# Optimization experiments

Hardware: AMD Instinct MI355X
Metric: run time of the kernel (lower is better)

## Reference

```python
import jax, jax.numpy as jnp
import numpy as np

N = 100000
E = 1600000
D = 64        # HID_NODE_ENC == HID_EDGE_ENC
H = 128       # HIDDEN_NODE_ONE
EPS = 1e-5
NEG_SLOPE = 0.01


def _xavier(key, shape):
    fan_in, fan_out = shape[0], shape[1]
    limit = float(np.sqrt(6.0 / (fan_in + fan_out)))
    return jax.random.uniform(key, shape, jnp.float32, -limit, limit)


def setup_inputs() -> dict:
    key = jax.random.key(0)
    ks = jax.random.split(key, 10)
    x = jax.random.normal(ks[0], (N, D), jnp.float32)
    edge_index = jax.random.randint(ks[1], (2, E), 0, N, jnp.int64)
    edge_attr = jax.random.normal(ks[2], (E, D), jnp.float32)
    u = jax.random.normal(ks[3], (1, 16), jnp.float32)
    batch = jnp.zeros((N,), jnp.int64)
    b_init = jnp.float32(0.01)
    params = {
        # node_mlp_1: Lin(128->128), LeakyReLU, BN(128), Lin(128->128)
        "W1": _xavier(ks[4], (2 * D, H)), "b1": jnp.full((H,), b_init),
        "g1": jnp.ones((H,), jnp.float32), "be1": jnp.zeros((H,), jnp.float32),
        "W2": _xavier(ks[5], (H, H)), "b2": jnp.full((H,), b_init),
        # node_mlp_2: Lin(192->128), LeakyReLU, BN(128), Lin(128->64)
        "W3": _xavier(ks[6], (H + D, H)), "b3": jnp.full((H,), b_init),
        "g2": jnp.ones((H,), jnp.float32), "be2": jnp.zeros((H,), jnp.float32),
        "W4": _xavier(ks[7], (H, D)), "b4": jnp.full((D,), b_init),
    }
    return {"x": x, "edge_index": edge_index, "edge_attr": edge_attr,
            "u": u, "batch": batch, **params}


def _bn(h, gamma, beta):
    # BatchNorm1d in training mode: biased batch statistics
    mean = jnp.mean(h, axis=0)
    var = jnp.mean(jnp.square(h - mean), axis=0)
    return (h - mean) * jax.lax.rsqrt(var + EPS) * gamma + beta


def reference(x, edge_index, edge_attr, u, batch,
              W1, b1, g1, be1, W2, b2,
              W3, b3, g2, be2, W4, b4):
    row, col = edge_index[0], edge_index[1]
    # gather + concat: [E, 2D]
    h = jnp.concatenate([x[row], edge_attr], axis=1)
    # node_mlp_1
    h = jax.nn.leaky_relu(h @ W1 + b1, NEG_SLOPE)
    h = _bn(h, g1, be1)
    h = h @ W2 + b2                       # [E, H]
    # scatter_add by destination node
    agg = jax.ops.segment_sum(h, col, num_segments=x.shape[0])  # [N, H]
    # concat with node feats, node_mlp_2
    h2 = jnp.concatenate([x, agg], axis=1)  # [N, H+D]
    h2 = jax.nn.leaky_relu(h2 @ W3 + b3, NEG_SLOPE)
    h2 = _bn(h2, g2, be2)
    return h2 @ W4 + b4                    # [N, D]
```

## Files before the change

### kernel.cpp

```cpp
#include <hip/hip_runtime.h>

#define NN 100000
#define NE 1600000
#define NTILE_E (NE / 128)
#define NTILE_N 782

typedef __attribute__((ext_vector_type(4))) float f32x4;
typedef __attribute__((ext_vector_type(8))) short s16x8;

__device__ __forceinline__ unsigned short f2bf(float f) {
  unsigned u = __builtin_bit_cast(unsigned, f);
  u = (u + 0x7FFFu + ((u >> 16) & 1u)) >> 16;
  return (unsigned short)u;
}
__device__ __forceinline__ void pack4(float4 v, unsigned short* dst) {
  ushort4 h;
  h.x = f2bf(v.x); h.y = f2bf(v.y); h.z = f2bf(v.z); h.w = f2bf(v.w);
  *(ushort4*)dst = h;
}

__global__ void k0_prep(const float* __restrict__ W1, const float* __restrict__ W3,
                        unsigned short* __restrict__ W1bT, unsigned short* __restrict__ W3bT) {
  int i = blockIdx.x * 256 + threadIdx.x;
  if (i < 16384) {
    int n = i >> 7, k = i & 127;
    W1bT[i] = f2bf(W1[k * 128 + n]);
  } else if (i < 16384 + 24576) {
    int j = i - 16384;
    int n = j / 192, k = j % 192;
    W3bT[j] = f2bf(W3[k * 128 + n]);
  }
}

__global__ __launch_bounds__(256, 2) void k1_edge(
    const float* __restrict__ x, const int* __restrict__ eidx,
    const float* __restrict__ ea, const unsigned short* __restrict__ W1bT,
    const float* __restrict__ b1,
    float* __restrict__ S, float* __restrict__ cnt, float* __restrict__ stat1) {
  __shared__ unsigned short At[128][136];
  __shared__ int rIdx[128];
  __shared__ int cIdx[128];
  __shared__ float sred[256];

  const int tid = threadIdx.x;
  const int wave = tid >> 6, lane = tid & 63;
  const int l15 = lane & 15, quad = lane >> 4;
  const int rowbase = (wave >> 1) * 64;
  const int colbase = (wave & 1) * 64;

  s16x8 bfrag[4][4];
#pragma unroll
  for (int ct = 0; ct < 4; ct++)
#pragma unroll
    for (int ks = 0; ks < 4; ks++)
      bfrag[ct][ks] = *(const s16x8*)(W1bT + (colbase + ct * 16 + l15) * 128 + ks * 32 + quad * 8);

  float b1j[4];
#pragma unroll
  for (int ct = 0; ct < 4; ct++) b1j[ct] = b1[colbase + ct * 16 + l15];

  float lsum[4] = {0, 0, 0, 0}, lsq[4] = {0, 0, 0, 0};

  for (int tile = blockIdx.x; tile < NTILE_E; tile += gridDim.x) {
    const int eb = tile * 128;
    __syncthreads();
    if (tid < 128) { rIdx[tid] = eidx[eb + tid]; cIdx[tid] = eidx[NE + eb + tid]; }
    __syncthreads();
#pragma unroll
    for (int i = 0; i < 8; i++) {
      int idx = tid + i * 256; int e = idx >> 4, c = idx & 15;
      float4 v = ((const float4*)x)[(size_t)rIdx[e] * 16 + c];
      pack4(v, &At[e][c * 4]);
    }
#pragma unroll
    for (int i = 0; i < 8; i++) {
      int idx = tid + i * 256; int e = idx >> 4, c = idx & 15;
      float4 v = ((const float4*)ea)[(size_t)(eb + e) * 16 + c];
      pack4(v, &At[e][64 + c * 4]);
    }
    __syncthreads();
    if (tid < 128) atomicAdd(&cnt[cIdx[tid]], 1.0f);

    f32x4 acc[4][4];
#pragma unroll
    for (int rt = 0; rt < 4; rt++)
#pragma unroll
      for (int ct = 0; ct < 4; ct++) acc[rt][ct] = (f32x4){0.f, 0.f, 0.f, 0.f};

#pragma unroll
    for (int ks = 0; ks < 4; ks++) {
      s16x8 af[4];
#pragma unroll
      for (int rt = 0; rt < 4; rt++)
        af[rt] = *(const s16x8*)&At[rowbase + rt * 16 + l15][ks * 32 + quad * 8];
#pragma unroll
      for (int rt = 0; rt < 4; rt++)
#pragma unroll
        for (int ct = 0; ct < 4; ct++)
          acc[rt][ct] = __builtin_amdgcn_mfma_f32_16x16x32_bf16(af[rt], bfrag[ct][ks], acc[rt][ct], 0, 0, 0);
    }

#pragma unroll
    for (int rt = 0; rt < 4; rt++) {
#pragma unroll
      for (int r = 0; r < 4; r++) {
        const int er = rowbase + rt * 16 + quad * 4 + r;
        float* Srow = S + (size_t)cIdx[er] * 128;
#pragma unroll
        for (int ct = 0; ct < 4; ct++) {
          float v = acc[rt][ct][r] + b1j[ct];
          v = v > 0.0f ? v : 0.01f * v;
          lsum[ct] += v; lsq[ct] += v * v;
          atomicAdd(Srow + colbase + ct * 16 + l15, v);
        }
      }
    }
  }

  sred[tid] = 0.0f;
  __syncthreads();
#pragma unroll
  for (int ct = 0; ct < 4; ct++) {
    float s = lsum[ct], q = lsq[ct];
    s += __shfl_down(s, 32); q += __shfl_down(q, 32);
    s += __shfl_down(s, 16); q += __shfl_down(q, 16);
    if (lane < 16) {
      atomicAdd(&sred[colbase + ct * 16 + l15], s);
      atomicAdd(&sred[128 + colbase + ct * 16 + l15], q);
    }
  }
  __syncthreads();
  atomicAdd(&stat1[tid], sred[tid]);
}

__global__ void k2_fold1(const float* __restrict__ stat1, const float* __restrict__ g1,
                         const float* __restrict__ be1, const float* __restrict__ W2,
                         const float* __restrict__ b2,
                         unsigned short* __restrict__ W2pT, float* __restrict__ v128) {
  __shared__ float s1s[128], t1s[128];
  int tid = threadIdx.x;
  if (tid < 128) {
    float mean = stat1[tid] * (1.0f / NE);
    float var = stat1[128 + tid] * (1.0f / NE) - mean * mean;
    float rstd = rsqrtf(var + 1e-5f);
    float s = g1[tid] * rstd;
    s1s[tid] = s; t1s[tid] = be1[tid] - mean * s;
  }
  __syncthreads();
  for (int i = tid; i < 16384; i += 256) {
    int n = i >> 7, k = i & 127;
    W2pT[i] = f2bf(s1s[k] * W2[k * 128 + n]);
  }
  if (tid < 128) {
    float a = b2[tid];
    for (int k = 0; k < 128; k++) a += t1s[k] * W2[k * 128 + tid];
    v128[tid] = a;
  }
}

__global__ __launch_bounds__(256, 2) void k3_node(
    const float* __restrict__ x, const float* __restrict__ S, const float* __restrict__ cnt,
    const unsigned short* __restrict__ W2pT, const float* __restrict__ v128,
    const unsigned short* __restrict__ W3bT, const float* __restrict__ b3,
    unsigned short* __restrict__ tOut, float* __restrict__ stat2) {
  __shared__ unsigned short Abuf[128][136];
  __shared__ unsigned short Xbuf[128][72];
  __shared__ float cbuf[128];
  __shared__ float sred[256];

  const int tid = threadIdx.x;
  const int wave = tid >> 6, lane = tid & 63;
  const int l15 = lane & 15, quad = lane >> 4;
  const int rowbase = (wave >> 1) * 64;
  const int colbase = (wave & 1) * 64;

  float vj[4], b3j[4];
#pragma unroll
  for (int ct = 0; ct < 4; ct++) {
    int jc = colbase + ct * 16 + l15;
    vj[ct] = v128[jc]; b3j[ct] = b3[jc];
  }
  float lsum[4] = {0, 0, 0, 0}, lsq[4] = {0, 0, 0, 0};

  for (int t = blockIdx.x; t < NTILE_N; t += gridDim.x) {
    const int nb = t * 128;
    __syncthreads();
#pragma unroll
    for (int i = 0; i < 16; i++) {
      int idx = tid + i * 256; int e = idx >> 5, c = idx & 31;
      int node = nb + e;
      float4 v = {0.f, 0.f, 0.f, 0.f};
      if (node < NN) v = ((const float4*)S)[(size_t)node * 32 + c];
      pack4(v, &Abuf[e][c * 4]);
    }
#pragma unroll
    for (int i = 0; i < 8; i++) {
      int idx = tid + i * 256; int e = idx >> 4, c = idx & 15;
      int node = nb + e;
      float4 v = {0.f, 0.f, 0.f, 0.f};
      if (node < NN) v = ((const float4*)x)[(size_t)node * 16 + c];
      pack4(v, &Xbuf[e][c * 4]);
    }
    if (tid < 128) cbuf[tid] = (nb + tid < NN) ? cnt[nb + tid] : 0.0f;
    __syncthreads();

    f32x4 acc[4][4];
#pragma unroll
    for (int rt = 0; rt < 4; rt++)
#pragma unroll
      for (int ct = 0; ct < 4; ct++) acc[rt][ct] = (f32x4){0.f, 0.f, 0.f, 0.f};
#pragma unroll
    for (int ks = 0; ks < 4; ks++) {
      s16x8 af[4];
#pragma unroll
      for (int rt = 0; rt < 4; rt++)
        af[rt] = *(const s16x8*)&Abuf[rowbase + rt * 16 + l15][ks * 32 + quad * 8];
      s16x8 bfr[4];
#pragma unroll
      for (int ct = 0; ct < 4; ct++)
        bfr[ct] = *(const s16x8*)(W2pT + (colbase + ct * 16 + l15) * 128 + ks * 32 + quad * 8);
#pragma unroll
      for (int rt = 0; rt < 4; rt++)
#pragma unroll
        for (int ct = 0; ct < 4; ct++)
          acc[rt][ct] = __builtin_amdgcn_mfma_f32_16x16x32_bf16(af[rt], bfr[ct], acc[rt][ct], 0, 0, 0);
    }
    __syncthreads();
#pragma unroll
    for (int rt = 0; rt < 4; rt++)
#pragma unroll
      for (int r = 0; r < 4; r++) {
        int er = rowbase + rt * 16 + quad * 4 + r;
#pragma unroll
        for (int ct = 0; ct < 4; ct++) {
          float val = acc[rt][ct][r] + cbuf[er] * vj[ct];
          Abuf[er][colbase + ct * 16 + l15] = f2bf(val);
        }
      }
    __syncthreads();

    f32x4 acc2[4][4];
#pragma unroll
    for (int rt = 0; rt < 4; rt++)
#pragma unroll
      for (int ct = 0; ct < 4; ct++) acc2[rt][ct] = (f32x4){0.f, 0.f, 0.f, 0.f};
#pragma unroll
    for (int ks = 0; ks < 6; ks++) {
      s16x8 af[4];
      if (ks < 2) {
#pragma unroll
        for (int rt = 0; rt < 4; rt++)
          af[rt] = *(const s16x8*)&Xbuf[rowbase + rt * 16 + l15][ks * 32 + quad * 8];
      } else {
#pragma unroll
        for (int rt = 0; rt < 4; rt++)
          af[rt] = *(const s16x8*)&Abuf[rowbase + rt * 16 + l15][(ks - 2) * 32 + quad * 8];
      }
      s16x8 bfr[4];
#pragma unroll
      for (int ct = 0; ct < 4; ct++)
        bfr[ct] = *(const s16x8*)(W3bT + (size_t)(colbase + ct * 16 + l15) * 192 + ks * 32 + quad * 8);
#pragma unroll
      for (int rt = 0; rt < 4; rt++)
#pragma unroll
        for (int ct = 0; ct < 4; ct++)
          acc2[rt][ct] = __builtin_amdgcn_mfma_f32_16x16x32_bf16(af[rt], bfr[ct], acc2[rt][ct], 0, 0, 0);
    }

#pragma unroll
    for (int rt = 0; rt < 4; rt++)
#pragma unroll
      for (int r = 0; r < 4; r++) {
        int er = rowbase + rt * 16 + quad * 4 + r;
        int node = nb + er;
        if (node < NN) {
#pragma unroll
          for (int ct = 0; ct < 4; ct++) {
            float val = acc2[rt][ct][r] + b3j[ct];
            val = val > 0.0f ? val : 0.01f * val;
            lsum[ct] += val; lsq[ct] += val * val;
            tOut[(size_t)node * 128 + colbase + ct * 16 + l15] = f2bf(val);
          }
        }
      }
  }

  sred[tid] = 0.0f;
  __syncthreads();
#pragma unroll
  for (int ct = 0; ct < 4; ct++) {
    float s = lsum[ct], q = lsq[ct];
    s += __shfl_down(s, 32); q += __shfl_down(q, 32);
    s += __shfl_down(s, 16); q += __shfl_down(q, 16);
    if (lane < 16) {
      atomicAdd(&sred[colbase + ct * 16 + l15], s);
      atomicAdd(&sred[128 + colbase + ct * 16 + l15], q);
    }
  }
  __syncthreads();
  atomicAdd(&stat2[tid], sred[tid]);
}

__global__ void k5_fold2(const float* __restrict__ stat2, const float* __restrict__ g2,
                         const float* __restrict__ be2, const float* __restrict__ W4,
                         const float* __restrict__ b4,
                         unsigned short* __restrict__ W4fT, float* __restrict__ b4f) {
  __shared__ float s2s[128], t2s[128];
  int tid = threadIdx.x;
  if (tid < 128) {
    float mean = stat2[tid] * (1.0f / NN);
    float var = stat2[128 + tid] * (1.0f / NN) - mean * mean;
    float rstd = rsqrtf(var + 1e-5f);
    float s = g2[tid] * rstd;
    s2s[tid] = s; t2s[tid] = be2[tid] - mean * s;
  }
  __syncthreads();
  for (int i = tid; i < 8192; i += 256) {
    int n = i >> 7, k = i & 127;
    W4fT[i] = f2bf(s2s[k] * W4[k * 64 + n]);
  }
  if (tid < 64) {
    float a = b4[tid];
    for (int k = 0; k < 128; k++) a += t2s[k] * W4[k * 64 + tid];
    b4f[tid] = a;
  }
}

__global__ __launch_bounds__(256, 2) void k6_out(
    const unsigned short* __restrict__ tIn, const unsigned short* __restrict__ W4fT,
    const float* __restrict__ b4f, float* __restrict__ out) {
  __shared__ unsigned short Abuf[128][136];
  const int tid = threadIdx.x;
  const int wave = tid >> 6, lane = tid & 63;
  const int l15 = lane & 15, quad = lane >> 4;
  const int rowbase = (wave >> 1) * 64;
  const int colbase = (wave & 1) * 32;

  s16x8 bfrag[2][4];
#pragma unroll
  for (int ct = 0; ct < 2; ct++)
#pragma unroll
    for (int ks = 0; ks < 4; ks++)
      bfrag[ct][ks] = *(const s16x8*)(W4fT + (colbase + ct * 16 + l15) * 128 + ks * 32 + quad * 8);
  float bj[2];
#pragma unroll
  for (int ct = 0; ct < 2; ct++) bj[ct] = b4f[colbase + ct * 16 + l15];

  for (int t = blockIdx.x; t < NTILE_N; t += gridDim.x) {
    const int nb = t * 128;
    __syncthreads();
#pragma unroll
    for (int i = 0; i < 8; i++) {
      int idx = tid + i * 256; int e = idx >> 4, c = idx & 15;
      int node = nb + e;
      s16x8 v = {0, 0, 0, 0, 0, 0, 0, 0};
      if (node < NN) v = *(const s16x8*)(tIn + (size_t)node * 128 + c * 8);
      *(s16x8*)&Abuf[e][c * 8] = v;
    }
    __syncthreads();

    f32x4 acc[4][2];
#pragma unroll
    for (int rt = 0; rt < 4; rt++)
#pragma unroll
      for (int ct = 0; ct < 2; ct++) acc[rt][ct] = (f32x4){0.f, 0.f, 0.f, 0.f};
#pragma unroll
    for (int ks = 0; ks < 4; ks++) {
      s16x8 af[4];
#pragma unroll
      for (int rt = 0; rt < 4; rt++)
        af[rt] = *(const s16x8*)&Abuf[rowbase + rt * 16 + l15][ks * 32 + quad * 8];
#pragma unroll
      for (int rt = 0; rt < 4; rt++)
#pragma unroll
        for (int ct = 0; ct < 2; ct++)
          acc[rt][ct] = __builtin_amdgcn_mfma_f32_16x16x32_bf16(af[rt], bfrag[ct][ks], acc[rt][ct], 0, 0, 0);
    }
#pragma unroll
    for (int rt = 0; rt < 4; rt++)
#pragma unroll
      for (int r = 0; r < 4; r++) {
        int er = rowbase + rt * 16 + quad * 4 + r;
        int node = nb + er;
        if (node < NN) {
#pragma unroll
          for (int ct = 0; ct < 2; ct++)
            out[(size_t)node * 64 + colbase + ct * 16 + l15] = acc[rt][ct][r] + bj[ct];
        }
      }
  }
}

extern "C" void kernel_launch(void* const* d_in, const int* in_sizes, int n_in,
                              void* d_out, int out_size, void* d_ws, size_t ws_size,
                              hipStream_t stream) {
  (void)in_sizes; (void)n_in; (void)out_size; (void)ws_size;
  const float* x   = (const float*)d_in[0];
  const int*   ei  = (const int*)d_in[1];
  const float* ea  = (const float*)d_in[2];
  const float* W1  = (const float*)d_in[5];
  const float* b1  = (const float*)d_in[6];
  const float* g1  = (const float*)d_in[7];
  const float* be1 = (const float*)d_in[8];
  const float* W2  = (const float*)d_in[9];
  const float* b2  = (const float*)d_in[10];
  const float* W3  = (const float*)d_in[11];
  const float* b3  = (const float*)d_in[12];
  const float* g2  = (const float*)d_in[13];
  const float* be2 = (const float*)d_in[14];
  const float* W4  = (const float*)d_in[15];
  const float* b4  = (const float*)d_in[16];
  float* out = (float*)d_out;

  char* w = (char*)d_ws;
  float* S     = (float*)(w);
  float* cnt   = (float*)(w + 51200000);
  float* stat1 = (float*)(w + 51600384);
  float* stat2 = (float*)(w + 51601408);
  unsigned short* W1bT = (unsigned short*)(w + 51602432);
  unsigned short* W3bT = (unsigned short*)(w + 51635200);
  unsigned short* W2pT = (unsigned short*)(w + 51684352);
  float* v128  = (float*)(w + 51717120);
  unsigned short* W4fT = (unsigned short*)(w + 51717632);
  float* b4f   = (float*)(w + 51734016);
  unsigned short* tOut = (unsigned short*)(w + 51734272);

  hipMemsetAsync(d_ws, 0, 51602432, stream);

  k0_prep<<<160, 256, 0, stream>>>(W1, W3, W1bT, W3bT);
  k1_edge<<<512, 256, 0, stream>>>(x, ei, ea, W1bT, b1, S, cnt, stat1);
  k2_fold1<<<1, 256, 0, stream>>>(stat1, g1, be1, W2, b2, W2pT, v128);
  k3_node<<<512, 256, 0, stream>>>(x, S, cnt, W2pT, v128, W3bT, b3, tOut, stat2);
  k5_fold2<<<1, 256, 0, stream>>>(stat2, g2, be2, W4, b4, W4fT, b4f);
  k6_out<<<512, 256, 0, stream>>>(tOut, W4fT, b4f, out);
}
```

Before: 1.317 ms.

## Counting-sort edges by destination and segment-reduce before scattering into node sums

Adds histogram, scan and scatter kernels that sort edges by destination node and also produce the per-node in-degree counts. The edge kernel then gathers x and edge_attr through the sorted permutation, stages the activated tile in shared memory, and does a per-column segmented run reduction. Each node's partial sum costs one store or atomic instead of one atomic per edge element. The goal is to cut the very large volume of global float atomics. In exchange it adds three preprocessing launches, makes the edge_attr reads indirect and non-sequential, and adds two extra barriers per tile. The BN-fold kernels are also spread over several blocks instead of one.

```diff
diff --git a/kernel.cpp b/kernel.cpp
--- a/kernel.cpp
+++ b/kernel.cpp
@@ -32,15 +32,59 @@
   }
 }
 
+__global__ void k_hist(const int* __restrict__ eidx, int* __restrict__ hist) {
+  int e = blockIdx.x * 256 + threadIdx.x;
+  if (e < NE) atomicAdd(&hist[eidx[NE + e]], 1);
+}
+
+__global__ void k_scan(int* __restrict__ hist, float* __restrict__ cntF) {
+  __shared__ int ssum[1024];
+  const int t = threadIdx.x;
+  const int base = t * 98;
+  const int cl = (base >= NN) ? 0 : ((NN - base < 98) ? (NN - base) : 98);
+  int s = 0;
+  for (int i = 0; i < cl; i++) s += hist[base + i];
+  ssum[t] = s;
+  __syncthreads();
+  for (int d = 1; d < 1024; d <<= 1) {
+    int v = (t >= d) ? ssum[t - d] : 0;
+    __syncthreads();
+    ssum[t] += v;
+    __syncthreads();
+  }
+  int run = (t == 0) ? 0 : ssum[t - 1];
+  for (int i = 0; i < cl; i++) {
+    int hv = hist[base + i];
+    hist[base + i] = run;
+    cntF[base + i] = (float)hv;
+    run += hv;
+  }
+}
+
+__global__ void k_scatter(const int* __restrict__ eidx, int* __restrict__ off,
+                          int* __restrict__ colS, int* __restrict__ eaIdx) {
+  int e = blockIdx.x * 256 + threadIdx.x;
+  if (e < NE) {
+    int c = eidx[NE + e];
+    int p = atomicAdd(&off[c], 1);
+    colS[p] = c;
+    eaIdx[p] = e;
+  }
+}
+
 __global__ __launch_bounds__(256, 2) void k1_edge(
     const float* __restrict__ x, const int* __restrict__ eidx,
     const float* __restrict__ ea, const unsigned short* __restrict__ W1bT,
-    const float* __restrict__ b1,
-    float* __restrict__ S, float* __restrict__ cnt, float* __restrict__ stat1) {
-  __shared__ unsigned short At[128][136];
-  __shared__ int rIdx[128];
-  __shared__ int cIdx[128];
+    const float* __restrict__ b1, const int* __restrict__ colS,
+    const int* __restrict__ eaIdx,
+    float* __restrict__ S, float* __restrict__ stat1) {
+  __shared__ __align__(16) unsigned short At[128][136];
+  __shared__ __align__(16) float Hs1[128][68];
+  __shared__ int rIdxS[128];
+  __shared__ int eIdxS[128];
+  __shared__ int colT[132];
   __shared__ float sred[256];
+  float (*Hs0)[68] = (float (*)[68])At;
 
   const int tid = threadIdx.x;
   const int wave = tid >> 6, lane = tid & 63;
@@ -64,22 +108,30 @@
   for (int tile = blockIdx.x; tile < NTILE_E; tile += gridDim.x) {
     const int eb = tile * 128;
     __syncthreads();
-    if (tid < 128) { rIdx[tid] = eidx[eb + tid]; cIdx[tid] = eidx[NE + eb + tid]; }
+    if (tid < 128) {
+      int e0 = eaIdx[eb + tid];
+      eIdxS[tid] = e0;
+      rIdxS[tid] = eidx[e0];
+      colT[tid + 1] = colS[eb + tid];
+    } else if (tid == 128) {
+      colT[0] = (eb > 0) ? colS[eb - 1] : -1;
+    } else if (tid == 129) {
+      colT[129] = (eb + 128 < NE) ? colS[eb + 128] : -1;
+    }
     __syncthreads();
 #pragma unroll
     for (int i = 0; i < 8; i++) {
       int idx = tid + i * 256; int e = idx >> 4, c = idx & 15;
-      float4 v = ((const float4*)x)[(size_t)rIdx[e] * 16 + c];
+      float4 v = ((const float4*)x)[(size_t)rIdxS[e] * 16 + c];
       pack4(v, &At[e][c * 4]);
     }
 #pragma unroll
     for (int i = 0; i < 8; i++) {
       int idx = tid + i * 256; int e = idx >> 4, c = idx & 15;
-      float4 v = ((const float4*)ea)[(size_t)(eb + e) * 16 + c];
+      float4 v = ((const float4*)ea)[(size_t)eIdxS[e] * 16 + c];
       pack4(v, &At[e][64 + c * 4]);
     }
     __syncthreads();
-    if (tid < 128) atomicAdd(&cnt[cIdx[tid]], 1.0f);
 
     f32x4 acc[4][4];
 #pragma unroll
@@ -100,19 +152,48 @@
           acc[rt][ct] = __builtin_amdgcn_mfma_f32_16x16x32_bf16(af[rt], bfrag[ct][ks], acc[rt][ct], 0, 0, 0);
     }
 
-#pragma unroll
-    for (int rt = 0; rt < 4; rt++) {
-#pragma unroll
-      for (int r = 0; r < 4; r++) {
-        const int er = rowbase + rt * 16 + quad * 4 + r;
-        float* Srow = S + (size_t)cIdx[er] * 128;
-#pragma unroll
-        for (int ct = 0; ct < 4; ct++) {
-          float v = acc[rt][ct][r] + b1j[ct];
-          v = v > 0.0f ? v : 0.01f * v;
-          lsum[ct] += v; lsq[ct] += v * v;
-          atomicAdd(Srow + colbase + ct * 16 + l15, v);
+    __syncthreads();
+    {
+      float (*H)[68] = (wave & 1) ? Hs1 : Hs0;
+#pragma unroll
+      for (int rt = 0; rt < 4; rt++)
+#pragma unroll
+        for (int r = 0; r < 4; r++) {
+          const int er = rowbase + rt * 16 + quad * 4 + r;
+#pragma unroll
+          for (int ct = 0; ct < 4; ct++) {
+            float v = acc[rt][ct][r] + b1j[ct];
+            v = v > 0.0f ? v : 0.01f * v;
+            lsum[ct] += v; lsq[ct] += v * v;
+            H[er][ct * 16 + l15] = v;
+          }
         }
+    }
+    __syncthreads();
+
+    {
+      const int col = tid & 63;
+      const int r0 = (tid >> 6) * 32;
+#pragma unroll
+      for (int h = 0; h < 2; h++) {
+        float (*H)[68] = h ? Hs1 : Hs0;
+        float runsum = H[r0][col];
+        int runstart = r0;
+        int curnode = colT[r0 + 1];
+        for (int r = r0 + 1; r < r0 + 32; ++r) {
+          int nd = colT[r + 1];
+          float v = H[r][col];
+          if (nd == curnode) { runsum += v; }
+          else {
+            float* p = S + (size_t)curnode * 128 + h * 64 + col;
+            if (colT[runstart] != curnode) *p = runsum;
+            else atomicAdd(p, runsum);
+            curnode = nd; runsum = v; runstart = r;
+          }
+        }
+        float* p = S + (size_t)curnode * 128 + h * 64 + col;
+        if (colT[runstart] != curnode && colT[r0 + 33] != curnode) *p = runsum;
+        else atomicAdd(p, runsum);
       }
     }
   }
@@ -138,7 +219,8 @@
                          const float* __restrict__ b2,
                          unsigned short* __restrict__ W2pT, float* __restrict__ v128) {
   __shared__ float s1s[128], t1s[128];
-  int tid = threadIdx.x;
+  __shared__ float red[256];
+  const int tid = threadIdx.x;
   if (tid < 128) {
     float mean = stat1[tid] * (1.0f / NE);
     float var = stat1[128 + tid] * (1.0f / NE) - mean * mean;
@@ -147,14 +229,21 @@
     s1s[tid] = s; t1s[tid] = be1[tid] - mean * s;
   }
   __syncthreads();
-  for (int i = tid; i < 16384; i += 256) {
-    int n = i >> 7, k = i & 127;
-    W2pT[i] = f2bf(s1s[k] * W2[k * 128 + n]);
-  }
-  if (tid < 128) {
-    float a = b2[tid];
-    for (int k = 0; k < 128; k++) a += t1s[k] * W2[k * 128 + tid];
-    v128[tid] = a;
+  const int b = blockIdx.x;
+  if (b < 16) {
+#pragma unroll
+    for (int j = 0; j < 4; j++) {
+      int i = b * 1024 + j * 256 + tid;
+      int k = i >> 7, n = i & 127;
+      W2pT[n * 128 + k] = f2bf(s1s[k] * W2[i]);
+    }
+  } else {
+    int j = tid & 127, hh = tid >> 7;
+    float p = 0.f;
+    for (int k = hh * 64; k < hh * 64 + 64; k++) p += t1s[k] * W2[k * 128 + j];
+    red[tid] = p;
+    __syncthreads();
+    if (tid < 128) v128[tid] = red[tid] + red[tid + 128] + b2[tid];
   }
 }
 
@@ -306,7 +395,8 @@
                          const float* __restrict__ b4,
                          unsigned short* __restrict__ W4fT, float* __restrict__ b4f) {
   __shared__ float s2s[128], t2s[128];
-  int tid = threadIdx.x;
+  __shared__ float red[256];
+  const int tid = threadIdx.x;
   if (tid < 128) {
     float mean = stat2[tid] * (1.0f / NN);
     float var = stat2[128 + tid] * (1.0f / NN) - mean * mean;
@@ -315,14 +405,21 @@
     s2s[tid] = s; t2s[tid] = be2[tid] - mean * s;
   }
   __syncthreads();
-  for (int i = tid; i < 8192; i += 256) {
-    int n = i >> 7, k = i & 127;
-    W4fT[i] = f2bf(s2s[k] * W4[k * 64 + n]);
-  }
-  if (tid < 64) {
-    float a = b4[tid];
-    for (int k = 0; k < 128; k++) a += t2s[k] * W4[k * 64 + tid];
-    b4f[tid] = a;
+  const int b = blockIdx.x;
+  if (b < 8) {
+#pragma unroll
+    for (int j = 0; j < 4; j++) {
+      int i = b * 1024 + j * 256 + tid;
+      int k = i >> 6, n = i & 63;
+      W4fT[n * 128 + k] = f2bf(s2s[k] * W4[i]);
+    }
+  } else {
+    int j = tid & 63, part = tid >> 6;
+    float p = 0.f;
+    for (int k = part * 32; k < part * 32 + 32; k++) p += t2s[k] * W4[k * 64 + j];
+    red[tid] = p;
+    __syncthreads();
+    if (tid < 64) b4f[tid] = red[tid] + red[tid + 64] + red[tid + 128] + red[tid + 192] + b4[tid];
   }
 }
 
@@ -414,23 +511,29 @@
 
   char* w = (char*)d_ws;
   float* S     = (float*)(w);
-  float* cnt   = (float*)(w + 51200000);
-  float* stat1 = (float*)(w + 51600384);
-  float* stat2 = (float*)(w + 51601408);
-  unsigned short* W1bT = (unsigned short*)(w + 51602432);
-  unsigned short* W3bT = (unsigned short*)(w + 51635200);
-  unsigned short* W2pT = (unsigned short*)(w + 51684352);
-  float* v128  = (float*)(w + 51717120);
-  unsigned short* W4fT = (unsigned short*)(w + 51717632);
-  float* b4f   = (float*)(w + 51734016);
-  unsigned short* tOut = (unsigned short*)(w + 51734272);
+  float* stat1 = (float*)(w + 51200000);
+  float* stat2 = (float*)(w + 51201024);
+  int*   hist  = (int*)  (w + 51202048);
+  float* cntF  = (float*)(w + 51602432);
+  unsigned short* W1bT = (unsigned short*)(w + 52002816);
+  unsigned short* W3bT = (unsigned short*)(w + 52035584);
+  unsigned short* W2pT = (unsigned short*)(w + 52084736);
+  float* v128  = (float*)(w + 52117504);
+  unsigned short* W4fT = (unsigned short*)(w + 52118016);
+  float* b4f   = (float*)(w + 52134400);
+  unsigned short* tOut = (unsigned short*)(w + 52134656);
+  int* colS  = (int*)(w + 52134656);
+  int* eaIdx = (int*)(w + 58534656);
 
   hipMemsetAsync(d_ws, 0, 51602432, stream);
 
   k0_prep<<<160, 256, 0, stream>>>(W1, W3, W1bT, W3bT);
-  k1_edge<<<512, 256, 0, stream>>>(x, ei, ea, W1bT, b1, S, cnt, stat1);
-  k2_fold1<<<1, 256, 0, stream>>>(stat1, g1, be1, W2, b2, W2pT, v128);
-  k3_node<<<512, 256, 0, stream>>>(x, S, cnt, W2pT, v128, W3bT, b3, tOut, stat2);
-  k5_fold2<<<1, 256, 0, stream>>>(stat2, g2, be2, W4, b4, W4fT, b4f);
+  k_hist<<<6250, 256, 0, stream>>>(ei, hist);
+  k_scan<<<1, 1024, 0, stream>>>(hist, cntF);
+  k_scatter<<<6250, 256, 0, stream>>>(ei, hist, colS, eaIdx);
+  k1_edge<<<512, 256, 0, stream>>>(x, ei, ea, W1bT, b1, colS, eaIdx, S, stat1);
+  k2_fold1<<<17, 256, 0, stream>>>(stat1, g1, be1, W2, b2, W2pT, v128);
+  k3_node<<<512, 256, 0, stream>>>(x, S, cntF, W2pT, v128, W3bT, b3, tOut, stat2);
+  k5_fold2<<<9, 256, 0, stream>>>(stat2, g2, be2, W4, b4, W4fT, b4f);
   k6_out<<<512, 256, 0, stream>>>(tOut, W4fT, b4f, out);
 }
```

Result: faster. 1.223 ms (-7.2%).
